# Kernel tuning notes

Measured on AMD Instinct MI355X. Metric: run time of the kernel, lower is better.

Reference implementation:

```python
import jax, jax.numpy as jnp
import numpy as np

B, C, E = 2, 128, 60000

def conv1(x, W, b):
    # pointwise conv1d: x [B,Cin,E], W [Cout,Cin], b [Cout] -> [B,Cout,E]
    return jnp.einsum('oc,bce->boe', W, x) + b[None, :, None]

def mesh_conv(x, gi, W, b):
    # MeshCNN GeMM conv: x [B,C,E], gi [B,E,4] neighbor edge ids, W [Cout,Cin,5], b [Cout]
    f = jax.vmap(lambda xb, ib: xb[:, ib])(x, gi)  # [B,C,E,4] neighbor gather
    f1, f2, f3, f4 = f[..., 0], f[..., 1], f[..., 2], f[..., 3]
    # symmetric features: [e, a+c, b+d, |a-c|, |b-d|]
    G = jnp.stack([x, f1 + f3, f2 + f4, jnp.abs(f1 - f3), jnp.abs(f2 - f4)], axis=-1)  # [B,C,E,5]
    return jnp.einsum('bces,ocs->boe', G, W) + b[None, :, None]


def setup_inputs() -> dict:
    key = jax.random.key(0)
    ks = jax.random.split(key, 16)
    s = 0.05
    return {
        'x_0': jax.random.normal(ks[0], (B, C, E), jnp.float32),
        'x_1': jax.random.normal(ks[1], (B, C, E), jnp.float32),
        'gemm': jax.random.randint(ks[2], (B, E, 4), 0, E, jnp.int32),
        'Wa_local': jax.random.normal(ks[3], (C, C), jnp.float32) * s,
        'ba_local': jax.random.normal(ks[4], (C,), jnp.float32) * s,
        'Wb_local': jax.random.normal(ks[5], (C, C), jnp.float32) * s,
        'bb_local': jax.random.normal(ks[6], (C,), jnp.float32) * s,
        'Wa_tri': jax.random.normal(ks[7], (C, C, 5), jnp.float32) * s,
        'ba_tri': jax.random.normal(ks[8], (C,), jnp.float32) * s,
        'Wb_tri': jax.random.normal(ks[9], (C, C, 5), jnp.float32) * s,
        'bb_tri': jax.random.normal(ks[10], (C,), jnp.float32) * s,
        'Wa_fuse': jax.random.normal(ks[11], (3, 2 * C), jnp.float32) * s,
        'ba_fuse': jax.random.normal(ks[12], (3,), jnp.float32) * s,
        'Wb_fuse': jax.random.normal(ks[13], (3, 2 * C), jnp.float32) * s,
        'bb_fuse': jax.random.normal(ks[14], (3,), jnp.float32) * s,
    }


def reference(x_0, x_1, gemm, Wa_local, ba_local, Wb_local, bb_local,
              Wa_tri, ba_tri, Wb_tri, bb_tri,
              Wa_fuse, ba_fuse, Wb_fuse, bb_fuse):
    a_local = conv1(x_0, Wa_local, ba_local)              # [B,C,E]
    a_tri = mesh_conv(x_0, gemm, Wa_tri, ba_tri)          # [B,C,E]
    x_a_two = jnp.concatenate([a_local, a_tri], axis=1)   # [B,2C,E]
    b_local = conv1(x_1, Wb_local, bb_local)
    b_tri = mesh_conv(x_1, gemm, Wb_tri, bb_tri)
    x_b_two = jnp.concatenate([b_local, b_tri], axis=1)
    x_a_w = conv1(x_a_two, Wa_fuse, ba_fuse)[:, None]     # [B,1,3,E]
    x_b_w = conv1(x_b_two, Wb_fuse, bb_fuse)[:, None]     # [B,1,3,E]
    return x_a_w + x_b_w
```

## Files before the change

### kernel.cpp

```cpp
#include <hip/hip_runtime.h>
#include <hip/hip_bf16.h>
#include <cstdint>

#define B_ 2
#define C_ 128
#define E_ 60000

typedef unsigned int uint32_;
typedef unsigned short ushort_;
typedef float v2f __attribute__((ext_vector_type(2)));
typedef float v4f __attribute__((ext_vector_type(4)));

__device__ __forceinline__ v2f bp2(uint32_ v) {
    v2f r;
    r.x = __uint_as_float(v << 16);
    r.y = __uint_as_float(v & 0xffff0000u);
    return r;
}

__device__ __forceinline__ v4f bp4(uint2 v) {
    v4f r;
    r.x = __uint_as_float(v.x << 16);
    r.y = __uint_as_float(v.x & 0xffff0000u);
    r.z = __uint_as_float(v.y << 16);
    r.w = __uint_as_float(v.y & 0xffff0000u);
    return r;
}

__device__ __forceinline__ v4f vabs4(v4f a) {
    v4f r; r.x = fabsf(a.x); r.y = fabsf(a.y); r.z = fabsf(a.z); r.w = fabsf(a.w);
    return r;
}

__device__ __forceinline__ ushort_ f2b(float f) {
    union { float f; uint32_ u; } x; x.f = f;
    uint32_ u = x.u + 0x7fffu + ((x.u >> 16) & 1u);
    return (ushort_)(u >> 16);
}

__device__ __forceinline__ float swz_add(float v, const int pat) {
    switch (pat) {
    case 1:  return v + __int_as_float(__builtin_amdgcn_ds_swizzle(__float_as_int(v), 0x041F));
    case 2:  return v + __int_as_float(__builtin_amdgcn_ds_swizzle(__float_as_int(v), 0x081F));
    case 4:  return v + __int_as_float(__builtin_amdgcn_ds_swizzle(__float_as_int(v), 0x101F));
    case 8:  return v + __int_as_float(__builtin_amdgcn_ds_swizzle(__float_as_int(v), 0x201F));
    default: return v + __int_as_float(__builtin_amdgcn_ds_swizzle(__float_as_int(v), 0x401F));
    }
}

__global__ __launch_bounds__(256) void prep_kernel(
    const float* __restrict__ x0, const float* __restrict__ x1,
    const float* __restrict__ Wa_local, const float* __restrict__ ba_local,
    const float* __restrict__ Wb_local, const float* __restrict__ bb_local,
    const float* __restrict__ Wa_tri,  const float* __restrict__ ba_tri,
    const float* __restrict__ Wb_tri,  const float* __restrict__ bb_tri,
    const float* __restrict__ Wa_fuse, const float* __restrict__ ba_fuse,
    const float* __restrict__ Wb_fuse, const float* __restrict__ bb_fuse,
    ushort_* __restrict__ xt, float* __restrict__ Vw, float* __restrict__ cst)
{
    __shared__ float smem[32 * 65];
    const int lane = threadIdx.x & 63;
    const int wv   = threadIdx.x >> 6;

    if (blockIdx.x < 60) {
        const int pj    = blockIdx.x / 10;
        const int chunk = blockIdx.x % 10;
        const int p = pj / 3, j = pj % 3;
        const int f = chunk * 64 + lane;
        const float* Wf = p ? Wb_fuse : Wa_fuse;
        const float* Wt = p ? Wb_tri  : Wa_tri;
        const float* Wl = p ? Wb_local : Wa_local;
        const int o0 = wv * 32;
        float a0 = 0.f, a1 = 0.f, a2 = 0.f, a3 = 0.f;
        for (int o = o0; o < o0 + 32; o += 4) {
            a0 += Wf[j * 256 + 128 + o]     * Wt[(o)     * 640 + f];
            a1 += Wf[j * 256 + 129 + o]     * Wt[(o + 1) * 640 + f];
            a2 += Wf[j * 256 + 130 + o]     * Wt[(o + 2) * 640 + f];
            a3 += Wf[j * 256 + 131 + o]     * Wt[(o + 3) * 640 + f];
        }
        float acc = (a0 + a1) + (a2 + a3);
        const int s = f % 5, c = f / 5;
        if (s == 0) {
            float b0 = 0.f, b1 = 0.f, b2 = 0.f, b3 = 0.f;
            for (int o = o0; o < o0 + 32; o += 4) {
                b0 += Wf[j * 256 + o]     * Wl[(o)     * C_ + c];
                b1 += Wf[j * 256 + o + 1] * Wl[(o + 1) * C_ + c];
                b2 += Wf[j * 256 + o + 2] * Wl[(o + 2) * C_ + c];
                b3 += Wf[j * 256 + o + 3] * Wl[(o + 3) * C_ + c];
            }
            acc += (b0 + b1) + (b2 + b3);
        }
        smem[wv * 64 + lane] = acc;
        __syncthreads();
        if (wv == 0) {
            float tot = smem[lane] + smem[64 + lane] + smem[128 + lane] + smem[192 + lane];
            Vw[(pj * 5 + s) * C_ + c] = tot;
        }
    } else if (blockIdx.x == 60) {
        const int j = wv;
        if (j < 3) {
            float acc;
            {
                const int l = lane;
                acc = Wa_fuse[j * 256 + l]       * ba_local[l]
                    + Wa_fuse[j * 256 + 128 + l] * ba_tri[l]
                    + Wb_fuse[j * 256 + l]       * bb_local[l]
                    + Wb_fuse[j * 256 + 128 + l] * bb_tri[l];
            }
            {
                const int l = lane + 64;
                acc += Wa_fuse[j * 256 + l]       * ba_local[l]
                     + Wa_fuse[j * 256 + 128 + l] * ba_tri[l]
                     + Wb_fuse[j * 256 + l]       * bb_local[l]
                     + Wb_fuse[j * 256 + 128 + l] * bb_tri[l];
            }
            acc = swz_add(acc, 1); acc = swz_add(acc, 2); acc = swz_add(acc, 4);
            acc = swz_add(acc, 8); acc = swz_add(acc, 16);
            acc += __shfl_xor(acc, 32, 64);
            if (lane == 0) cst[j] = acc + ba_fuse[j] + bb_fuse[j];
        }
    } else {
        const int tb = blockIdx.x - 61;
        const int bx = tb % 1875;
        const int rz = tb / 1875;
        const int by = rz & 1;
        const int bz = rz >> 1;
        const int which = bz >> 1;
        const int b     = bz & 1;
        const float* src = (which ? x1 : x0) + (size_t)b * C_ * E_;
        const int e0 = bx * 32;
        const int c0 = by * 64;
        const int t  = threadIdx.x;
        float (*tile)[65] = (float(*)[65])smem;
        {
            const int c  = t >> 2;
            const int e8 = (t & 3) * 8;
            const float* pp = src + (size_t)(c0 + c) * E_ + e0 + e8;
            float4 v0 = *(const float4*)pp;
            float4 v1 = *(const float4*)(pp + 4);
            tile[e8 + 0][c] = v0.x; tile[e8 + 1][c] = v0.y;
            tile[e8 + 2][c] = v0.z; tile[e8 + 3][c] = v0.w;
            tile[e8 + 4][c] = v1.x; tile[e8 + 5][c] = v1.y;
            tile[e8 + 6][c] = v1.z; tile[e8 + 7][c] = v1.w;
        }
        __syncthreads();
        {
            const int e  = t >> 3;
            const int c8 = (t & 7) * 8;
            const float* r = &tile[e][c8];
            uint32_ w0 = (uint32_)f2b(r[0]) | ((uint32_)f2b(r[1]) << 16);
            uint32_ w1 = (uint32_)f2b(r[2]) | ((uint32_)f2b(r[3]) << 16);
            uint32_ w2 = (uint32_)f2b(r[4]) | ((uint32_)f2b(r[5]) << 16);
            uint32_ w3 = (uint32_)f2b(r[6]) | ((uint32_)f2b(r[7]) << 16);
            uint4 w; w.x = w0; w.y = w1; w.z = w2; w.w = w3;
            const size_t rec = (size_t)((b * E_ + e0 + e) * 2 + which);
            *(uint4*)(xt + (rec << 7) + c0 + c8) = w;
        }
    }
}

__global__ __launch_bounds__(256, 4) void mesh_fused_kernel(
    const uint2* __restrict__ xt2, const int* __restrict__ gemm,
    const float* __restrict__ Vw, const float* __restrict__ cst,
    float* __restrict__ out)
{
    const int lane = threadIdx.x & 63;
    const int wv   = threadIdx.x >> 6;
    const int gw   = blockIdx.x * 4 + wv;
    const int nw   = gridDim.x * 4;

    const int p  = lane >> 5;
    const int c4 = (lane & 31) * 4;
    v4f w[3][5];
#pragma unroll
    for (int j = 0; j < 3; ++j)
#pragma unroll
        for (int s = 0; s < 5; ++s)
            w[j][s] = *(const v4f*)(Vw + ((p * 3 + j) * 5 + s) * C_ + c4);

    const int  jj     = lane >> 4;
    const bool is0    = (jj == 0), is1 = (jj == 1);
    const bool writer = ((lane & 15) == 0) && (jj < 3);
    const float cj    = is0 ? cst[0] : (is1 ? cst[1] : cst[2]);
    float* obase      = out + (size_t)(jj < 3 ? jj : 2) * E_;

    const int4* g4 = (const int4*)gemm;
    const int npair = (B_ * E_) / 2;

    int4 giA = g4[2 * gw], giB = g4[2 * gw + 1];

    for (int pair = gw; pair < npair; pair += nw) {
        const int nxt = pair + nw;
        const int4 gA = giA, gB = giB;
        if (nxt < npair) { giA = g4[2 * nxt]; giB = g4[2 * nxt + 1]; }

        const int e0 = 2 * pair;
        const uint32_ badd = (e0 >= E_) ? (uint32_)E_ : 0u;

        const uint2 SA = xt2[(((uint32_)e0)     << 6) + lane];
        const uint2 SB = xt2[(((uint32_)e0 + 1) << 6) + lane];
        const uint2 A1 = xt2[((badd + (uint32_)gA.x) << 6) + lane];
        const uint2 A2 = xt2[((badd + (uint32_)gA.y) << 6) + lane];
        const uint2 A3 = xt2[((badd + (uint32_)gA.z) << 6) + lane];
        const uint2 A4 = xt2[((badd + (uint32_)gA.w) << 6) + lane];
        const uint2 B1 = xt2[((badd + (uint32_)gB.x) << 6) + lane];
        const uint2 B2 = xt2[((badd + (uint32_)gB.y) << 6) + lane];
        const uint2 B3 = xt2[((badd + (uint32_)gB.z) << 6) + lane];
        const uint2 B4 = xt2[((badd + (uint32_)gB.w) << 6) + lane];

        float rA0, rA1, rA2;
        {
            v4f a0 = bp4(SA);
            v4f a1 = bp4(A1), a2 = bp4(A2), a3 = bp4(A3), a4 = bp4(A4);
            v4f s1 = a1 + a3, s2 = a2 + a4;
            v4f d1 = vabs4(a1 - a3), d2 = vabs4(a2 - a4);
            v4f t0 = w[0][0] * a0, t1 = w[1][0] * a0, t2 = w[2][0] * a0;
            t0 += w[0][1] * s1; t1 += w[1][1] * s1; t2 += w[2][1] * s1;
            t0 += w[0][2] * s2; t1 += w[1][2] * s2; t2 += w[2][2] * s2;
            t0 += w[0][3] * d1; t1 += w[1][3] * d1; t2 += w[2][3] * d1;
            t0 += w[0][4] * d2; t1 += w[1][4] * d2; t2 += w[2][4] * d2;
            rA0 = (t0.x + t0.y) + (t0.z + t0.w);
            rA1 = (t1.x + t1.y) + (t1.z + t1.w);
            rA2 = (t2.x + t2.y) + (t2.z + t2.w);
        }
        float rB0, rB1, rB2;
        {
            v4f a0 = bp4(SB);
            v4f a1 = bp4(B1), a2 = bp4(B2), a3 = bp4(B3), a4 = bp4(B4);
            v4f s1 = a1 + a3, s2 = a2 + a4;
            v4f d1 = vabs4(a1 - a3), d2 = vabs4(a2 - a4);
            v4f t0 = w[0][0] * a0, t1 = w[1][0] * a0, t2 = w[2][0] * a0;
            t0 += w[0][1] * s1; t1 += w[1][1] * s1; t2 += w[2][1] * s1;
            t0 += w[0][2] * s2; t1 += w[1][2] * s2; t2 += w[2][2] * s2;
            t0 += w[0][3] * d1; t1 += w[1][3] * d1; t2 += w[2][3] * d1;
            t0 += w[0][4] * d2; t1 += w[1][4] * d2; t2 += w[2][4] * d2;
            rB0 = (t0.x + t0.y) + (t0.z + t0.w);
            rB1 = (t1.x + t1.y) + (t1.z + t1.w);
            rB2 = (t2.x + t2.y) + (t2.z + t2.w);
        }

        rA0 = swz_add(rA0, 16); rB0 = swz_add(rB0, 16);
        rA1 = swz_add(rA1, 16); rB1 = swz_add(rB1, 16);
        rA2 = swz_add(rA2, 16); rB2 = swz_add(rB2, 16);
        rA0 += __shfl_xor(rA0, 32, 64); rB0 += __shfl_xor(rB0, 32, 64);
        rA1 += __shfl_xor(rA1, 32, 64); rB1 += __shfl_xor(rB1, 32, 64);
        rA2 += __shfl_xor(rA2, 32, 64); rB2 += __shfl_xor(rB2, 32, 64);

        float vA = is0 ? rA0 : (is1 ? rA1 : rA2);
        float vB = is0 ? rB0 : (is1 ? rB1 : rB2);
        vA = swz_add(vA, 1); vB = swz_add(vB, 1);
        vA = swz_add(vA, 2); vB = swz_add(vB, 2);
        vA = swz_add(vA, 4); vB = swz_add(vB, 4);
        vA = swz_add(vA, 8); vB = swz_add(vB, 8);

        if (writer) {
            const int bb = (e0 >= E_) ? 1 : 0;
            const int ee = e0 - (bb ? E_ : 0);
            float2 st; st.x = vA + cj; st.y = vB + cj;
            *(float2*)(obase + (bb ? 3 * E_ : 0) + ee) = st;
        }
    }
}

extern "C" void kernel_launch(void* const* d_in, const int* in_sizes, int n_in,
                              void* d_out, int out_size, void* d_ws, size_t ws_size,
                              hipStream_t stream) {
    const float* x0       = (const float*)d_in[0];
    const float* x1       = (const float*)d_in[1];
    const int*   gemm     = (const int*)d_in[2];
    const float* Wa_local = (const float*)d_in[3];
    const float* ba_local = (const float*)d_in[4];
    const float* Wb_local = (const float*)d_in[5];
    const float* bb_local = (const float*)d_in[6];
    const float* Wa_tri   = (const float*)d_in[7];
    const float* ba_tri   = (const float*)d_in[8];
    const float* Wb_tri   = (const float*)d_in[9];
    const float* bb_tri   = (const float*)d_in[10];
    const float* Wa_fuse  = (const float*)d_in[11];
    const float* ba_fuse  = (const float*)d_in[12];
    const float* Wb_fuse  = (const float*)d_in[13];
    const float* bb_fuse  = (const float*)d_in[14];
    float* out = (float*)d_out;

    ushort_* xt  = (ushort_*)d_ws;
    float*   Vw  = (float*)(xt + (size_t)B_ * E_ * 2 * C_);
    float*   cst = Vw + 2 * 3 * 5 * C_;

    hipLaunchKernelGGL(prep_kernel, dim3(61 + 8 * (E_ / 32)), dim3(256), 0, stream,
                       x0, x1,
                       Wa_local, ba_local, Wb_local, bb_local,
                       Wa_tri, ba_tri, Wb_tri, bb_tri,
                       Wa_fuse, ba_fuse, Wb_fuse, bb_fuse, xt, Vw, cst);

    hipLaunchKernelGGL(mesh_fused_kernel, dim3(2048), dim3(256), 0, stream,
                       (const uint2*)xt, gemm, Vw, cst, out);
}
```

Baseline: 213.6 us.

## Compute center-edge term in transpose kernel, split weight folding into own kernel

Weight folding moves into a separate small kernel. The transpose/convert kernel now also computes the per-edge center-feature contribution (s=0 term) from the bf16 tile in LDS and writes it to a y0 buffer. The mesh kernel no longer loads the center edge records; it reads y0 instead, which cuts one gather-stream record per edge and trims the register weights from 15 to 12 vectors. The cost is an extra kernel launch, an extra serialization point, and y0 write/read traffic. The LDS tile now uses an XOR swizzle over a 64-edge by 256-channel layout.

```diff
diff --git a/kernel.cpp b/kernel.cpp
--- a/kernel.cpp
+++ b/kernel.cpp
@@ -10,13 +10,6 @@
 typedef unsigned short ushort_;
 typedef float v2f __attribute__((ext_vector_type(2)));
 typedef float v4f __attribute__((ext_vector_type(4)));
-
-__device__ __forceinline__ v2f bp2(uint32_ v) {
-    v2f r;
-    r.x = __uint_as_float(v << 16);
-    r.y = __uint_as_float(v & 0xffff0000u);
-    return r;
-}
 
 __device__ __forceinline__ v4f bp4(uint2 v) {
     v4f r;
@@ -48,17 +41,16 @@
     }
 }
 
-__global__ __launch_bounds__(256) void prep_kernel(
-    const float* __restrict__ x0, const float* __restrict__ x1,
+__global__ __launch_bounds__(256) void fold_kernel(
     const float* __restrict__ Wa_local, const float* __restrict__ ba_local,
     const float* __restrict__ Wb_local, const float* __restrict__ bb_local,
     const float* __restrict__ Wa_tri,  const float* __restrict__ ba_tri,
     const float* __restrict__ Wb_tri,  const float* __restrict__ bb_tri,
     const float* __restrict__ Wa_fuse, const float* __restrict__ ba_fuse,
     const float* __restrict__ Wb_fuse, const float* __restrict__ bb_fuse,
-    ushort_* __restrict__ xt, float* __restrict__ Vw, float* __restrict__ cst)
+    float* __restrict__ Vw, float* __restrict__ cst)
 {
-    __shared__ float smem[32 * 65];
+    __shared__ float smem[256];
     const int lane = threadIdx.x & 63;
     const int wv   = threadIdx.x >> 6;
 
@@ -96,7 +88,7 @@
             float tot = smem[lane] + smem[64 + lane] + smem[128 + lane] + smem[192 + lane];
             Vw[(pj * 5 + s) * C_ + c] = tot;
         }
-    } else if (blockIdx.x == 60) {
+    } else {
         const int j = wv;
         if (j < 3) {
             float acc;
@@ -119,50 +111,99 @@
             acc += __shfl_xor(acc, 32, 64);
             if (lane == 0) cst[j] = acc + ba_fuse[j] + bb_fuse[j];
         }
-    } else {
-        const int tb = blockIdx.x - 61;
-        const int bx = tb % 1875;
-        const int rz = tb / 1875;
-        const int by = rz & 1;
-        const int bz = rz >> 1;
-        const int which = bz >> 1;
-        const int b     = bz & 1;
-        const float* src = (which ? x1 : x0) + (size_t)b * C_ * E_;
-        const int e0 = bx * 32;
-        const int c0 = by * 64;
-        const int t  = threadIdx.x;
-        float (*tile)[65] = (float(*)[65])smem;
-        {
-            const int c  = t >> 2;
-            const int e8 = (t & 3) * 8;
-            const float* pp = src + (size_t)(c0 + c) * E_ + e0 + e8;
-            float4 v0 = *(const float4*)pp;
-            float4 v1 = *(const float4*)(pp + 4);
-            tile[e8 + 0][c] = v0.x; tile[e8 + 1][c] = v0.y;
-            tile[e8 + 2][c] = v0.z; tile[e8 + 3][c] = v0.w;
-            tile[e8 + 4][c] = v1.x; tile[e8 + 5][c] = v1.y;
-            tile[e8 + 6][c] = v1.z; tile[e8 + 7][c] = v1.w;
-        }
-        __syncthreads();
-        {
-            const int e  = t >> 3;
-            const int c8 = (t & 7) * 8;
-            const float* r = &tile[e][c8];
-            uint32_ w0 = (uint32_)f2b(r[0]) | ((uint32_)f2b(r[1]) << 16);
-            uint32_ w1 = (uint32_)f2b(r[2]) | ((uint32_)f2b(r[3]) << 16);
-            uint32_ w2 = (uint32_)f2b(r[4]) | ((uint32_)f2b(r[5]) << 16);
-            uint32_ w3 = (uint32_)f2b(r[6]) | ((uint32_)f2b(r[7]) << 16);
-            uint4 w; w.x = w0; w.y = w1; w.z = w2; w.w = w3;
-            const size_t rec = (size_t)((b * E_ + e0 + e) * 2 + which);
-            *(uint4*)(xt + (rec << 7) + c0 + c8) = w;
-        }
-    }
-}
-
-__global__ __launch_bounds__(256, 4) void mesh_fused_kernel(
+    }
+}
+
+__device__ __forceinline__ int lds_off(int e, int row) {
+    return e * 264 + (((row >> 3) ^ ((e >> 3) & 7)) << 3) + (row & 7);
+}
+
+__global__ __launch_bounds__(256) void prep_kernel(
+    const float* __restrict__ x0, const float* __restrict__ x1,
+    const float* __restrict__ Vw,
+    ushort_* __restrict__ xt, float* __restrict__ y0)
+{
+    __shared__ __align__(16) ushort_ tile[64 * 264];
+    __shared__ float wsm[768];
+    const int t = threadIdx.x;
+    const int l = t & 63;
+    const int w = t >> 6;
+    const int b  = blockIdx.y;
+    const int e0 = blockIdx.x * 64;
+    const int nvalid = min(64, E_ - e0);
+
+    for (int f = t; f < 768; f += 256) {
+        const int p = f / 384, rem = f - p * 384;
+        const int j = rem >> 7, c = rem & 127;
+        wsm[f] = Vw[((p * 3 + j) * 5) * C_ + c];
+    }
+
+    const int rowi = t >> 4;
+    const int e4   = (t & 15) * 4;
+    const bool rdok = e4 < nvalid;
+#pragma unroll
+    for (int r = 0; r < 16; ++r) {
+        const int row = r * 16 + rowi;
+        const int p = row >> 7, c = row & 127;
+        if (rdok) {
+            const float* src = (p ? x1 : x0) + ((size_t)b * C_ + c) * E_ + e0 + e4;
+            float4 v = *(const float4*)src;
+            tile[lds_off(e4 + 0, row)] = f2b(v.x);
+            tile[lds_off(e4 + 1, row)] = f2b(v.y);
+            tile[lds_off(e4 + 2, row)] = f2b(v.z);
+            tile[lds_off(e4 + 3, row)] = f2b(v.w);
+        }
+    }
+    __syncthreads();
+
+#pragma unroll
+    for (int k = 0; k < 8; ++k) {
+        const int rec = w * 16 + k * 2 + (l >> 5);
+        const int g   = l & 31;
+        const uint4 vv = *(const uint4*)(tile + rec * 264 + ((g ^ ((rec >> 3) & 7)) << 3));
+        if (rec < nvalid)
+            *(uint4*)(xt + ((size_t)(b * E_ + e0 + rec) << 8) + g * 8) = vv;
+    }
+
+    {
+        const int e = t >> 2, q = t & 3;
+        const int p = q >> 1;
+        const int xr = (e >> 3) & 7;
+        float a0 = 0.f, a1 = 0.f, a2 = 0.f;
+        const float* w0 = wsm + p * 384;
+        const float* w1 = w0 + 128;
+        const float* w2 = w1 + 128;
+#pragma unroll
+        for (int i = 0; i < 8; ++i) {
+            const int grp = q * 8 + i;
+            const uint4 u = *(const uint4*)(tile + e * 264 + ((grp ^ xr) << 3));
+            const int cb = (q & 1) * 64 + i * 8;
+            const uint32_ uu[4] = {u.x, u.y, u.z, u.w};
+#pragma unroll
+            for (int m = 0; m < 4; ++m) {
+                const float flo = __uint_as_float(uu[m] << 16);
+                const float fhi = __uint_as_float(uu[m] & 0xffff0000u);
+                const int c = cb + 2 * m;
+                a0 += w0[c] * flo + w0[c + 1] * fhi;
+                a1 += w1[c] * flo + w1[c + 1] * fhi;
+                a2 += w2[c] * flo + w2[c + 1] * fhi;
+            }
+        }
+        a0 = swz_add(a0, 1); a1 = swz_add(a1, 1); a2 = swz_add(a2, 1);
+        a0 = swz_add(a0, 2); a1 = swz_add(a1, 2); a2 = swz_add(a2, 2);
+        if (q == 0 && e < nvalid) {
+            const size_t eb = (size_t)b * 3 * E_ + e0 + e;
+            y0[eb]          = a0;
+            y0[eb + E_]     = a1;
+            y0[eb + 2 * E_] = a2;
+        }
+    }
+}
+
+__global__ __launch_bounds__(256, 4) void mesh_kernel(
     const uint2* __restrict__ xt2, const int* __restrict__ gemm,
     const float* __restrict__ Vw, const float* __restrict__ cst,
-    float* __restrict__ out)
+    const float* __restrict__ y0, float* __restrict__ out)
 {
     const int lane = threadIdx.x & 63;
     const int wv   = threadIdx.x >> 6;
@@ -171,18 +212,19 @@
 
     const int p  = lane >> 5;
     const int c4 = (lane & 31) * 4;
-    v4f w[3][5];
+    v4f w[3][4];
 #pragma unroll
     for (int j = 0; j < 3; ++j)
 #pragma unroll
-        for (int s = 0; s < 5; ++s)
-            w[j][s] = *(const v4f*)(Vw + ((p * 3 + j) * 5 + s) * C_ + c4);
+        for (int s = 1; s < 5; ++s)
+            w[j][s - 1] = *(const v4f*)(Vw + ((p * 3 + j) * 5 + s) * C_ + c4);
 
     const int  jj     = lane >> 4;
+    const int  jjc    = jj < 3 ? jj : 2;
     const bool is0    = (jj == 0), is1 = (jj == 1);
     const bool writer = ((lane & 15) == 0) && (jj < 3);
     const float cj    = is0 ? cst[0] : (is1 ? cst[1] : cst[2]);
-    float* obase      = out + (size_t)(jj < 3 ? jj : 2) * E_;
+    float* obase      = out + (size_t)jjc * E_;
 
     const int4* g4 = (const int4*)gemm;
     const int npair = (B_ * E_) / 2;
@@ -195,10 +237,10 @@
         if (nxt < npair) { giA = g4[2 * nxt]; giB = g4[2 * nxt + 1]; }
 
         const int e0 = 2 * pair;
-        const uint32_ badd = (e0 >= E_) ? (uint32_)E_ : 0u;
-
-        const uint2 SA = xt2[(((uint32_)e0)     << 6) + lane];
-        const uint2 SB = xt2[(((uint32_)e0 + 1) << 6) + lane];
+        const int bb = (e0 >= E_) ? 1 : 0;
+        const uint32_ badd = bb ? (uint32_)E_ : 0u;
+        const int ee = e0 - (int)badd;
+
         const uint2 A1 = xt2[((badd + (uint32_)gA.x) << 6) + lane];
         const uint2 A2 = xt2[((badd + (uint32_)gA.y) << 6) + lane];
         const uint2 A3 = xt2[((badd + (uint32_)gA.z) << 6) + lane];
@@ -207,33 +249,30 @@
         const uint2 B2 = xt2[((badd + (uint32_)gB.y) << 6) + lane];
         const uint2 B3 = xt2[((badd + (uint32_)gB.z) << 6) + lane];
         const uint2 B4 = xt2[((badd + (uint32_)gB.w) << 6) + lane];
+        const float2 yj = *(const float2*)(y0 + ((size_t)bb * 3 + jjc) * E_ + ee);
 
         float rA0, rA1, rA2;
         {
-            v4f a0 = bp4(SA);
             v4f a1 = bp4(A1), a2 = bp4(A2), a3 = bp4(A3), a4 = bp4(A4);
             v4f s1 = a1 + a3, s2 = a2 + a4;
             v4f d1 = vabs4(a1 - a3), d2 = vabs4(a2 - a4);
-            v4f t0 = w[0][0] * a0, t1 = w[1][0] * a0, t2 = w[2][0] * a0;
-            t0 += w[0][1] * s1; t1 += w[1][1] * s1; t2 += w[2][1] * s1;
-            t0 += w[0][2] * s2; t1 += w[1][2] * s2; t2 += w[2][2] * s2;
-            t0 += w[0][3] * d1; t1 += w[1][3] * d1; t2 += w[2][3] * d1;
-            t0 += w[0][4] * d2; t1 += w[1][4] * d2; t2 += w[2][4] * d2;
+            v4f t0 = w[0][0] * s1, t1 = w[1][0] * s1, t2 = w[2][0] * s1;
+            t0 += w[0][1] * s2; t1 += w[1][1] * s2; t2 += w[2][1] * s2;
+            t0 += w[0][2] * d1; t1 += w[1][2] * d1; t2 += w[2][2] * d1;
+            t0 += w[0][3] * d2; t1 += w[1][3] * d2; t2 += w[2][3] * d2;
             rA0 = (t0.x + t0.y) + (t0.z + t0.w);
             rA1 = (t1.x + t1.y) + (t1.z + t1.w);
             rA2 = (t2.x + t2.y) + (t2.z + t2.w);
         }
         float rB0, rB1, rB2;
         {
-            v4f a0 = bp4(SB);
             v4f a1 = bp4(B1), a2 = bp4(B2), a3 = bp4(B3), a4 = bp4(B4);
             v4f s1 = a1 + a3, s2 = a2 + a4;
             v4f d1 = vabs4(a1 - a3), d2 = vabs4(a2 - a4);
-            v4f t0 = w[0][0] * a0, t1 = w[1][0] * a0, t2 = w[2][0] * a0;
-            t0 += w[0][1] * s1; t1 += w[1][1] * s1; t2 += w[2][1] * s1;
-            t0 += w[0][2] * s2; t1 += w[1][2] * s2; t2 += w[2][2] * s2;
-            t0 += w[0][3] * d1; t1 += w[1][3] * d1; t2 += w[2][3] * d1;
-            t0 += w[0][4] * d2; t1 += w[1][4] * d2; t2 += w[2][4] * d2;
+            v4f t0 = w[0][0] * s1, t1 = w[1][0] * s1, t2 = w[2][0] * s1;
+            t0 += w[0][1] * s2; t1 += w[1][1] * s2; t2 += w[2][1] * s2;
+            t0 += w[0][2] * d1; t1 += w[1][2] * d1; t2 += w[2][2] * d1;
+            t0 += w[0][3] * d2; t1 += w[1][3] * d2; t2 += w[2][3] * d2;
             rB0 = (t0.x + t0.y) + (t0.z + t0.w);
             rB1 = (t1.x + t1.y) + (t1.z + t1.w);
             rB2 = (t2.x + t2.y) + (t2.z + t2.w);
@@ -254,9 +293,7 @@
         vA = swz_add(vA, 8); vB = swz_add(vB, 8);
 
         if (writer) {
-            const int bb = (e0 >= E_) ? 1 : 0;
-            const int ee = e0 - (bb ? E_ : 0);
-            float2 st; st.x = vA + cj; st.y = vB + cj;
+            float2 st; st.x = vA + yj.x + cj; st.y = vB + yj.y + cj;
             *(float2*)(obase + (bb ? 3 * E_ : 0) + ee) = st;
         }
     }
@@ -283,15 +320,18 @@
     float* out = (float*)d_out;
 
     ushort_* xt  = (ushort_*)d_ws;
-    float*   Vw  = (float*)(xt + (size_t)B_ * E_ * 2 * C_);
+    float*   y0  = (float*)(xt + (size_t)B_ * E_ * 2 * C_);
+    float*   Vw  = y0 + (size_t)B_ * 3 * E_;
     float*   cst = Vw + 2 * 3 * 5 * C_;
 
-    hipLaunchKernelGGL(prep_kernel, dim3(61 + 8 * (E_ / 32)), dim3(256), 0, stream,
-                       x0, x1,
+    hipLaunchKernelGGL(fold_kernel, dim3(61), dim3(256), 0, stream,
                        Wa_local, ba_local, Wb_local, bb_local,
                        Wa_tri, ba_tri, Wb_tri, bb_tri,
-                       Wa_fuse, ba_fuse, Wb_fuse, bb_fuse, xt, Vw, cst);
-
-    hipLaunchKernelGGL(mesh_fused_kernel, dim3(2048), dim3(256), 0, stream,
-                       (const uint2*)xt, gemm, Vw, cst, out);
-}
+                       Wa_fuse, ba_fuse, Wb_fuse, bb_fuse, Vw, cst);
+
+    hipLaunchKernelGGL(prep_kernel, dim3((E_ + 63) / 64, B_), dim3(256), 0, stream,
+                       x0, x1, Vw, xt, y0);
+
+    hipLaunchKernelGGL(mesh_kernel, dim3(2048), dim3(256), 0, stream,
+                       (const uint2*)xt, gemm, Vw, cst, y0, out);
+}
```

After: 226.7 us. 1.06x slower.

## Split work per batch to overlap batch-1 transpose with batch-0 mesh conv

Applied to the files above, without the earlier changes.

Work is now split by batch across three kernels. Phase 1 builds the weights and transposes batch 0. Phase 2 runs the mesh conv for batch 0 in 256 blocks while the remaining blocks transpose batch 1. Phase 3 runs the mesh conv for batch 1. The goal is to overlap the bandwidth-heavy transpose with the gather-heavy mesh conv. The cost is an extra kernel launch and a fixed 256-block share for the batch-0 mesh work, which may be unbalanced against the transpose blocks.

```diff
diff --git a/kernel.cpp b/kernel.cpp
--- a/kernel.cpp
+++ b/kernel.cpp
@@ -5,18 +5,12 @@
 #define B_ 2
 #define C_ 128
 #define E_ 60000
+#define NTILE 1875
+#define NMESH2 256
 
 typedef unsigned int uint32_;
 typedef unsigned short ushort_;
-typedef float v2f __attribute__((ext_vector_type(2)));
 typedef float v4f __attribute__((ext_vector_type(4)));
-
-__device__ __forceinline__ v2f bp2(uint32_ v) {
-    v2f r;
-    r.x = __uint_as_float(v << 16);
-    r.y = __uint_as_float(v & 0xffff0000u);
-    return r;
-}
 
 __device__ __forceinline__ v4f bp4(uint2 v) {
     v4f r;
@@ -48,7 +42,147 @@
     }
 }
 
-__global__ __launch_bounds__(256) void prep_kernel(
+__device__ __forceinline__ void do_transpose(
+    int tb, int b, const float* __restrict__ x0, const float* __restrict__ x1,
+    ushort_* __restrict__ xt, float (*tile)[65])
+{
+    const int combo = tb / NTILE;
+    const int bx    = tb % NTILE;
+    const int by    = combo & 1;
+    const int which = combo >> 1;
+    const float* src = (which ? x1 : x0) + (size_t)b * C_ * E_;
+    const int e0 = bx * 32;
+    const int c0 = by * 64;
+    const int t  = threadIdx.x;
+    {
+        const int c  = t >> 2;
+        const int e8 = (t & 3) * 8;
+        const float* pp = src + (size_t)(c0 + c) * E_ + e0 + e8;
+        float4 v0 = *(const float4*)pp;
+        float4 v1 = *(const float4*)(pp + 4);
+        tile[e8 + 0][c] = v0.x; tile[e8 + 1][c] = v0.y;
+        tile[e8 + 2][c] = v0.z; tile[e8 + 3][c] = v0.w;
+        tile[e8 + 4][c] = v1.x; tile[e8 + 5][c] = v1.y;
+        tile[e8 + 6][c] = v1.z; tile[e8 + 7][c] = v1.w;
+    }
+    __syncthreads();
+    {
+        const int e  = t >> 3;
+        const int c8 = (t & 7) * 8;
+        const float* r = &tile[e][c8];
+        uint32_ w0 = (uint32_)f2b(r[0]) | ((uint32_)f2b(r[1]) << 16);
+        uint32_ w1 = (uint32_)f2b(r[2]) | ((uint32_)f2b(r[3]) << 16);
+        uint32_ w2 = (uint32_)f2b(r[4]) | ((uint32_)f2b(r[5]) << 16);
+        uint32_ w3 = (uint32_)f2b(r[6]) | ((uint32_)f2b(r[7]) << 16);
+        uint4 w; w.x = w0; w.y = w1; w.z = w2; w.w = w3;
+        const size_t rec = (size_t)((b * E_ + e0 + e) * 2 + which);
+        *(uint4*)(xt + (rec << 7) + c0 + c8) = w;
+    }
+}
+
+__device__ __forceinline__ void do_mesh(
+    int gw, int nw, int pair_lo, int pair_hi,
+    const uint2* __restrict__ xt2, const int* __restrict__ gemm,
+    const float* __restrict__ Vw, const float* __restrict__ cst,
+    float* __restrict__ out)
+{
+    const int lane = threadIdx.x & 63;
+
+    const int p  = lane >> 5;
+    const int c4 = (lane & 31) * 4;
+    v4f w[3][5];
+#pragma unroll
+    for (int j = 0; j < 3; ++j)
+#pragma unroll
+        for (int s = 0; s < 5; ++s)
+            w[j][s] = *(const v4f*)(Vw + ((p * 3 + j) * 5 + s) * C_ + c4);
+
+    const int  jj     = lane >> 4;
+    const bool is0    = (jj == 0), is1 = (jj == 1);
+    const bool writer = ((lane & 15) == 0) && (jj < 3);
+    const float cj    = is0 ? cst[0] : (is1 ? cst[1] : cst[2]);
+    float* obase      = out + (size_t)(jj < 3 ? jj : 2) * E_;
+
+    const int4* g4 = (const int4*)gemm;
+
+    const int p0 = pair_lo + gw;
+    if (p0 >= pair_hi) return;
+    int4 giA = g4[2 * p0], giB = g4[2 * p0 + 1];
+
+    for (int pair = p0; pair < pair_hi; pair += nw) {
+        const int nxt = pair + nw;
+        const int4 gA = giA, gB = giB;
+        if (nxt < pair_hi) { giA = g4[2 * nxt]; giB = g4[2 * nxt + 1]; }
+
+        const int e0 = 2 * pair;
+        const uint32_ badd = (e0 >= E_) ? (uint32_)E_ : 0u;
+
+        const uint2 SA = xt2[(((uint32_)e0)     << 6) + lane];
+        const uint2 SB = xt2[(((uint32_)e0 + 1) << 6) + lane];
+        const uint2 A1 = xt2[((badd + (uint32_)gA.x) << 6) + lane];
+        const uint2 A2 = xt2[((badd + (uint32_)gA.y) << 6) + lane];
+        const uint2 A3 = xt2[((badd + (uint32_)gA.z) << 6) + lane];
+        const uint2 A4 = xt2[((badd + (uint32_)gA.w) << 6) + lane];
+        const uint2 B1 = xt2[((badd + (uint32_)gB.x) << 6) + lane];
+        const uint2 B2 = xt2[((badd + (uint32_)gB.y) << 6) + lane];
+        const uint2 B3 = xt2[((badd + (uint32_)gB.z) << 6) + lane];
+        const uint2 B4 = xt2[((badd + (uint32_)gB.w) << 6) + lane];
+
+        float rA0, rA1, rA2;
+        {
+            v4f a0 = bp4(SA);
+            v4f a1 = bp4(A1), a2 = bp4(A2), a3 = bp4(A3), a4 = bp4(A4);
+            v4f s1 = a1 + a3, s2 = a2 + a4;
+            v4f d1 = vabs4(a1 - a3), d2 = vabs4(a2 - a4);
+            v4f t0 = w[0][0] * a0, t1 = w[1][0] * a0, t2 = w[2][0] * a0;
+            t0 += w[0][1] * s1; t1 += w[1][1] * s1; t2 += w[2][1] * s1;
+            t0 += w[0][2] * s2; t1 += w[1][2] * s2; t2 += w[2][2] * s2;
+            t0 += w[0][3] * d1; t1 += w[1][3] * d1; t2 += w[2][3] * d1;
+            t0 += w[0][4] * d2; t1 += w[1][4] * d2; t2 += w[2][4] * d2;
+            rA0 = (t0.x + t0.y) + (t0.z + t0.w);
+            rA1 = (t1.x + t1.y) + (t1.z + t1.w);
+            rA2 = (t2.x + t2.y) + (t2.z + t2.w);
+        }
+        float rB0, rB1, rB2;
+        {
+            v4f a0 = bp4(SB);
+            v4f a1 = bp4(B1), a2 = bp4(B2), a3 = bp4(B3), a4 = bp4(B4);
+            v4f s1 = a1 + a3, s2 = a2 + a4;
+            v4f d1 = vabs4(a1 - a3), d2 = vabs4(a2 - a4);
+            v4f t0 = w[0][0] * a0, t1 = w[1][0] * a0, t2 = w[2][0] * a0;
+            t0 += w[0][1] * s1; t1 += w[1][1] * s1; t2 += w[2][1] * s1;
+            t0 += w[0][2] * s2; t1 += w[1][2] * s2; t2 += w[2][2] * s2;
+            t0 += w[0][3] * d1; t1 += w[1][3] * d1; t2 += w[2][3] * d1;
+            t0 += w[0][4] * d2; t1 += w[1][4] * d2; t2 += w[2][4] * d2;
+            rB0 = (t0.x + t0.y) + (t0.z + t0.w);
+            rB1 = (t1.x + t1.y) + (t1.z + t1.w);
+            rB2 = (t2.x + t2.y) + (t2.z + t2.w);
+        }
+
+        rA0 = swz_add(rA0, 16); rB0 = swz_add(rB0, 16);
+        rA1 = swz_add(rA1, 16); rB1 = swz_add(rB1, 16);
+        rA2 = swz_add(rA2, 16); rB2 = swz_add(rB2, 16);
+        rA0 += __shfl_xor(rA0, 32, 64); rB0 += __shfl_xor(rB0, 32, 64);
+        rA1 += __shfl_xor(rA1, 32, 64); rB1 += __shfl_xor(rB1, 32, 64);
+        rA2 += __shfl_xor(rA2, 32, 64); rB2 += __shfl_xor(rB2, 32, 64);
+
+        float vA = is0 ? rA0 : (is1 ? rA1 : rA2);
+        float vB = is0 ? rB0 : (is1 ? rB1 : rB2);
+        vA = swz_add(vA, 1); vB = swz_add(vB, 1);
+        vA = swz_add(vA, 2); vB = swz_add(vB, 2);
+        vA = swz_add(vA, 4); vB = swz_add(vB, 4);
+        vA = swz_add(vA, 8); vB = swz_add(vB, 8);
+
+        if (writer) {
+            const int bb = (e0 >= E_) ? 1 : 0;
+            const int ee = e0 - (bb ? E_ : 0);
+            float2 st; st.x = vA + cj; st.y = vB + cj;
+            *(float2*)(obase + (bb ? 3 * E_ : 0) + ee) = st;
+        }
+    }
+}
+
+__global__ __launch_bounds__(256) void phase1_kernel(
     const float* __restrict__ x0, const float* __restrict__ x1,
     const float* __restrict__ Wa_local, const float* __restrict__ ba_local,
     const float* __restrict__ Wb_local, const float* __restrict__ bb_local,
@@ -58,11 +192,12 @@
     const float* __restrict__ Wb_fuse, const float* __restrict__ bb_fuse,
     ushort_* __restrict__ xt, float* __restrict__ Vw, float* __restrict__ cst)
 {
-    __shared__ float smem[32 * 65];
+    __shared__ float tile[32][65];
     const int lane = threadIdx.x & 63;
     const int wv   = threadIdx.x >> 6;
 
     if (blockIdx.x < 60) {
+        float* smemf = &tile[0][0];
         const int pj    = blockIdx.x / 10;
         const int chunk = blockIdx.x % 10;
         const int p = pj / 3, j = pj % 3;
@@ -90,10 +225,10 @@
             }
             acc += (b0 + b1) + (b2 + b3);
         }
-        smem[wv * 64 + lane] = acc;
+        smemf[wv * 64 + lane] = acc;
         __syncthreads();
         if (wv == 0) {
-            float tot = smem[lane] + smem[64 + lane] + smem[128 + lane] + smem[192 + lane];
+            float tot = smemf[lane] + smemf[64 + lane] + smemf[128 + lane] + smemf[192 + lane];
             Vw[(pj * 5 + s) * C_ + c] = tot;
         }
     } else if (blockIdx.x == 60) {
@@ -120,146 +255,34 @@
             if (lane == 0) cst[j] = acc + ba_fuse[j] + bb_fuse[j];
         }
     } else {
-        const int tb = blockIdx.x - 61;
-        const int bx = tb % 1875;
-        const int rz = tb / 1875;
-        const int by = rz & 1;
-        const int bz = rz >> 1;
-        const int which = bz >> 1;
-        const int b     = bz & 1;
-        const float* src = (which ? x1 : x0) + (size_t)b * C_ * E_;
-        const int e0 = bx * 32;
-        const int c0 = by * 64;
-        const int t  = threadIdx.x;
-        float (*tile)[65] = (float(*)[65])smem;
-        {
-            const int c  = t >> 2;
-            const int e8 = (t & 3) * 8;
-            const float* pp = src + (size_t)(c0 + c) * E_ + e0 + e8;
-            float4 v0 = *(const float4*)pp;
-            float4 v1 = *(const float4*)(pp + 4);
-            tile[e8 + 0][c] = v0.x; tile[e8 + 1][c] = v0.y;
-            tile[e8 + 2][c] = v0.z; tile[e8 + 3][c] = v0.w;
-            tile[e8 + 4][c] = v1.x; tile[e8 + 5][c] = v1.y;
-            tile[e8 + 6][c] = v1.z; tile[e8 + 7][c] = v1.w;
-        }
-        __syncthreads();
-        {
-            const int e  = t >> 3;
-            const int c8 = (t & 7) * 8;
-            const float* r = &tile[e][c8];
-            uint32_ w0 = (uint32_)f2b(r[0]) | ((uint32_)f2b(r[1]) << 16);
-            uint32_ w1 = (uint32_)f2b(r[2]) | ((uint32_)f2b(r[3]) << 16);
-            uint32_ w2 = (uint32_)f2b(r[4]) | ((uint32_)f2b(r[5]) << 16);
-            uint32_ w3 = (uint32_)f2b(r[6]) | ((uint32_)f2b(r[7]) << 16);
-            uint4 w; w.x = w0; w.y = w1; w.z = w2; w.w = w3;
-            const size_t rec = (size_t)((b * E_ + e0 + e) * 2 + which);
-            *(uint4*)(xt + (rec << 7) + c0 + c8) = w;
-        }
-    }
-}
-
-__global__ __launch_bounds__(256, 4) void mesh_fused_kernel(
-    const uint2* __restrict__ xt2, const int* __restrict__ gemm,
+        do_transpose(blockIdx.x - 61, 0, x0, x1, xt, tile);
+    }
+}
+
+__global__ __launch_bounds__(256, 4) void phase2_kernel(
+    const float* __restrict__ x0, const float* __restrict__ x1,
+    ushort_* __restrict__ xt, const int* __restrict__ gemm,
     const float* __restrict__ Vw, const float* __restrict__ cst,
     float* __restrict__ out)
 {
-    const int lane = threadIdx.x & 63;
-    const int wv   = threadIdx.x >> 6;
-    const int gw   = blockIdx.x * 4 + wv;
-    const int nw   = gridDim.x * 4;
-
-    const int p  = lane >> 5;
-    const int c4 = (lane & 31) * 4;
-    v4f w[3][5];
-#pragma unroll
-    for (int j = 0; j < 3; ++j)
-#pragma unroll
-        for (int s = 0; s < 5; ++s)
-            w[j][s] = *(const v4f*)(Vw + ((p * 3 + j) * 5 + s) * C_ + c4);
-
-    const int  jj     = lane >> 4;
-    const bool is0    = (jj == 0), is1 = (jj == 1);
-    const bool writer = ((lane & 15) == 0) && (jj < 3);
-    const float cj    = is0 ? cst[0] : (is1 ? cst[1] : cst[2]);
-    float* obase      = out + (size_t)(jj < 3 ? jj : 2) * E_;
-
-    const int4* g4 = (const int4*)gemm;
-    const int npair = (B_ * E_) / 2;
-
-    int4 giA = g4[2 * gw], giB = g4[2 * gw + 1];
-
-    for (int pair = gw; pair < npair; pair += nw) {
-        const int nxt = pair + nw;
-        const int4 gA = giA, gB = giB;
-        if (nxt < npair) { giA = g4[2 * nxt]; giB = g4[2 * nxt + 1]; }
-
-        const int e0 = 2 * pair;
-        const uint32_ badd = (e0 >= E_) ? (uint32_)E_ : 0u;
-
-        const uint2 SA = xt2[(((uint32_)e0)     << 6) + lane];
-        const uint2 SB = xt2[(((uint32_)e0 + 1) << 6) + lane];
-        const uint2 A1 = xt2[((badd + (uint32_)gA.x) << 6) + lane];
-        const uint2 A2 = xt2[((badd + (uint32_)gA.y) << 6) + lane];
-        const uint2 A3 = xt2[((badd + (uint32_)gA.z) << 6) + lane];
-        const uint2 A4 = xt2[((badd + (uint32_)gA.w) << 6) + lane];
-        const uint2 B1 = xt2[((badd + (uint32_)gB.x) << 6) + lane];
-        const uint2 B2 = xt2[((badd + (uint32_)gB.y) << 6) + lane];
-        const uint2 B3 = xt2[((badd + (uint32_)gB.z) << 6) + lane];
-        const uint2 B4 = xt2[((badd + (uint32_)gB.w) << 6) + lane];
-
-        float rA0, rA1, rA2;
-        {
-            v4f a0 = bp4(SA);
-            v4f a1 = bp4(A1), a2 = bp4(A2), a3 = bp4(A3), a4 = bp4(A4);
-            v4f s1 = a1 + a3, s2 = a2 + a4;
-            v4f d1 = vabs4(a1 - a3), d2 = vabs4(a2 - a4);
-            v4f t0 = w[0][0] * a0, t1 = w[1][0] * a0, t2 = w[2][0] * a0;
-            t0 += w[0][1] * s1; t1 += w[1][1] * s1; t2 += w[2][1] * s1;
-            t0 += w[0][2] * s2; t1 += w[1][2] * s2; t2 += w[2][2] * s2;
-            t0 += w[0][3] * d1; t1 += w[1][3] * d1; t2 += w[2][3] * d1;
-            t0 += w[0][4] * d2; t1 += w[1][4] * d2; t2 += w[2][4] * d2;
-            rA0 = (t0.x + t0.y) + (t0.z + t0.w);
-            rA1 = (t1.x + t1.y) + (t1.z + t1.w);
-            rA2 = (t2.x + t2.y) + (t2.z + t2.w);
-        }
-        float rB0, rB1, rB2;
-        {
-            v4f a0 = bp4(SB);
-            v4f a1 = bp4(B1), a2 = bp4(B2), a3 = bp4(B3), a4 = bp4(B4);
-            v4f s1 = a1 + a3, s2 = a2 + a4;
-            v4f d1 = vabs4(a1 - a3), d2 = vabs4(a2 - a4);
-            v4f t0 = w[0][0] * a0, t1 = w[1][0] * a0, t2 = w[2][0] * a0;
-            t0 += w[0][1] * s1; t1 += w[1][1] * s1; t2 += w[2][1] * s1;
-            t0 += w[0][2] * s2; t1 += w[1][2] * s2; t2 += w[2][2] * s2;
-            t0 += w[0][3] * d1; t1 += w[1][3] * d1; t2 += w[2][3] * d1;
-            t0 += w[0][4] * d2; t1 += w[1][4] * d2; t2 += w[2][4] * d2;
-            rB0 = (t0.x + t0.y) + (t0.z + t0.w);
-            rB1 = (t1.x + t1.y) + (t1.z + t1.w);
-            rB2 = (t2.x + t2.y) + (t2.z + t2.w);
-        }
-
-        rA0 = swz_add(rA0, 16); rB0 = swz_add(rB0, 16);
-        rA1 = swz_add(rA1, 16); rB1 = swz_add(rB1, 16);
-        rA2 = swz_add(rA2, 16); rB2 = swz_add(rB2, 16);
-        rA0 += __shfl_xor(rA0, 32, 64); rB0 += __shfl_xor(rB0, 32, 64);
-        rA1 += __shfl_xor(rA1, 32, 64); rB1 += __shfl_xor(rB1, 32, 64);
-        rA2 += __shfl_xor(rA2, 32, 64); rB2 += __shfl_xor(rB2, 32, 64);
-
-        float vA = is0 ? rA0 : (is1 ? rA1 : rA2);
-        float vB = is0 ? rB0 : (is1 ? rB1 : rB2);
-        vA = swz_add(vA, 1); vB = swz_add(vB, 1);
-        vA = swz_add(vA, 2); vB = swz_add(vB, 2);
-        vA = swz_add(vA, 4); vB = swz_add(vB, 4);
-        vA = swz_add(vA, 8); vB = swz_add(vB, 8);
-
-        if (writer) {
-            const int bb = (e0 >= E_) ? 1 : 0;
-            const int ee = e0 - (bb ? E_ : 0);
-            float2 st; st.x = vA + cj; st.y = vB + cj;
-            *(float2*)(obase + (bb ? 3 * E_ : 0) + ee) = st;
-        }
-    }
+    __shared__ float tile[32][65];
+    if (blockIdx.x < NMESH2) {
+        const int wv = threadIdx.x >> 6;
+        do_mesh(blockIdx.x * 4 + wv, NMESH2 * 4, 0, E_ / 2,
+                (const uint2*)xt, gemm, Vw, cst, out);
+    } else {
+        do_transpose(blockIdx.x - NMESH2, 1, x0, x1, xt, tile);
+    }
+}
+
+__global__ __launch_bounds__(256, 4) void phase3_kernel(
+    const ushort_* __restrict__ xt, const int* __restrict__ gemm,
+    const float* __restrict__ Vw, const float* __restrict__ cst,
+    float* __restrict__ out)
+{
+    const int wv = threadIdx.x >> 6;
+    do_mesh(blockIdx.x * 4 + wv, gridDim.x * 4, E_ / 2, E_,
+            (const uint2*)xt, gemm, Vw, cst, out);
 }
 
 extern "C" void kernel_launch(void* const* d_in, const int* in_sizes, int n_in,
@@ -286,12 +309,15 @@
     float*   Vw  = (float*)(xt + (size_t)B_ * E_ * 2 * C_);
     float*   cst = Vw + 2 * 3 * 5 * C_;
 
-    hipLaunchKernelGGL(prep_kernel, dim3(61 + 8 * (E_ / 32)), dim3(256), 0, stream,
+    hipLaunchKernelGGL(phase1_kernel, dim3(61 + 4 * NTILE), dim3(256), 0, stream,
                        x0, x1,
                        Wa_local, ba_local, Wb_local, bb_local,
                        Wa_tri, ba_tri, Wb_tri, bb_tri,
                        Wa_fuse, ba_fuse, Wb_fuse, bb_fuse, xt, Vw, cst);
 
-    hipLaunchKernelGGL(mesh_fused_kernel, dim3(2048), dim3(256), 0, stream,
-                       (const uint2*)xt, gemm, Vw, cst, out);
-}
+    hipLaunchKernelGGL(phase2_kernel, dim3(NMESH2 + 4 * NTILE), dim3(256), 0, stream,
+                       x0, x1, xt, gemm, Vw, cst, out);
+
+    hipLaunchKernelGGL(phase3_kernel, dim3(2048), dim3(256), 0, stream,
+                       xt, gemm, Vw, cst, out);
+}
```

Result: slower. 223.5 us (+4.7%).
